# Optimization experiments

Measured on AMD Instinct MI355X. Metric: run time of the kernel, lower is better.

The kernel has to match this reference:

```python
import jax, jax.numpy as jnp
import numpy as np

E = 8          # num_experts
D = 512        # embed_dim
FF = 4         # ff_mult
H = D * FF     # hidden
B, N = 4, 2048
TOP_K = 2


def setup_inputs() -> dict:
    key = jax.random.key(0)
    ks = jax.random.split(key, 6)
    tokens = jax.random.normal(ks[0], (B, N, D), dtype=jnp.float32)
    # token-choice top-k routing: logits -> top-2 experts per token
    logits = jax.random.normal(ks[1], (B, N, E), dtype=jnp.float32)
    topv, topi = jax.lax.top_k(logits, TOP_K)            # (B,N,K)
    disp = jnp.zeros((B, N, E), jnp.float32)
    disp = jnp.take_along_axis(disp, topi, axis=-1)  # placeholder shape trick avoided below
    disp = jnp.zeros((B, N, E), jnp.float32).at[
        jnp.arange(B)[:, None, None], jnp.arange(N)[None, :, None], topi
    ].set(1.0)                                            # (B,N,E) 0/1 dispatch mask
    w = jax.nn.softmax(topv, axis=-1)                     # combine weights over selected
    comb = jnp.zeros((B, N, E), jnp.float32).at[
        jnp.arange(B)[:, None, None], jnp.arange(N)[None, :, None], topi
    ].set(w)
    # expert params (xavier-ish scale); out_proj gain 0.02 as in module init
    Wg = jax.random.normal(ks[2], (E, D, H), dtype=jnp.float32) * (2.0 / (D + H)) ** 0.5
    Wv = jax.random.normal(ks[3], (E, D, H), dtype=jnp.float32) * (2.0 / (D + H)) ** 0.5
    Wo = jax.random.normal(ks[4], (E, H, D), dtype=jnp.float32) * 0.02 * (2.0 / (D + H)) ** 0.5
    scales = jnp.full((E,), 1.0 / E, dtype=jnp.float32)   # output_scale per expert
    return {"tokens": tokens, "dispatch_weights": disp, "combine_weights": comb,
            "Wg": Wg, "Wv": Wv, "Wo": Wo, "scales": scales}


def reference(tokens, dispatch_weights, combine_weights, Wg, Wv, Wo, scales):
    """ExpertPool.forward: per-expert SwiGLU FFN, combined by routing weights.

    Dense-masked formulation (same math as gather->FFN->weighted scatter-add:
    expert outputs only contribute where dispatch>0).
    """
    b, n, d = tokens.shape
    x = tokens.reshape(b * n, d)                          # (M, D)
    gate = jax.nn.gelu(jnp.einsum('md,edh->emh', x, Wg), approximate=False)
    value = jnp.einsum('md,edh->emh', x, Wv)
    out_e = jnp.einsum('emh,ehd->emd', gate * value, Wo) * scales[:, None, None]
    mask = dispatch_weights.reshape(b * n, -1) > 0        # (M, E)
    w = jnp.where(mask, combine_weights.reshape(b * n, -1), 0.0)
    out = jnp.einsum('emd,me->md', out_e, w)              # weighted combine
    return out.reshape(b, n, d)
```

## Files before the change

### kernel.cpp

```cpp
#include <hip/hip_runtime.h>
#include <hip/hip_bf16.h>


#define NEXP 8
#define DIM 512
#define HID 2048
#define MTOK 8192
#define PMAX (2*MTOK)
#define TM 128
#define MT 144

typedef __bf16 bf16;
typedef __bf16 bf16x8 __attribute__((ext_vector_type(8)));
typedef float  f32x4  __attribute__((ext_vector_type(4)));

#define WAITVM(N) asm volatile("s_waitcnt vmcnt(" #N ")" ::: "memory")
#define SCHED0    __builtin_amdgcn_sched_barrier(0)
#define BAR       __builtin_amdgcn_s_barrier

__device__ __forceinline__ void gload16(const bf16* g, bf16* l) {
  __builtin_amdgcn_global_load_lds(
      (const __attribute__((address_space(1))) void*)g,
      (__attribute__((address_space(3))) void*)l, 16, 0, 0);
}

__device__ __forceinline__ float gelu_f(float x){
  float s = x * 0.70710678118654752f;
  float a = fabsf(s);
  float t = 1.0f / fmaf(0.3275911f, a, 1.0f);
  float p = t*(0.254829592f + t*(-0.284496736f + t*(1.421413741f +
            t*(-1.453152027f + t*1.061405429f))));
  float er = 1.0f - p*__expf(-s*s);
  er = copysignf(er, s);
  return 0.5f*x*(1.0f + er);
}

__device__ __forceinline__ bool tile_map(const int* __restrict__ cnt, int T,
                                         int& row0, int& nrows) {
  int sb = 0, stt = 0; bool ok = false;
#pragma unroll
  for (int q=0; q<NEXP; q++){
    int c = cnt[q];
    int nt = (c + TM-1)/TM;
    if (!ok && T >= stt && T < stt+nt){
      int k = T - stt;
      row0 = sb + k*TM;
      int nr = c - k*TM; if (nr > TM) nr = TM;
      nrows = nr; ok = true;
    }
    stt += nt; sb += c;
  }
  return ok;
}

__global__ __launch_bounds__(256) void k_prep(
    const float* __restrict__ Wg, const float* __restrict__ Wv,
    const float* __restrict__ Wo,
    bf16* __restrict__ WgT, bf16* __restrict__ WvT, bf16* __restrict__ WoT,
    const float* __restrict__ disp, int* __restrict__ cnt) {
  __shared__ __align__(16) bf16 t[64][72];
  __shared__ int lc[NEXP];
  const int b = blockIdx.x, tid = threadIdx.x;

  if (b < 6144) {
    const float* pin; bf16* pout; int R, C, c0, r0;
    if (b < 4096) {
      int u = b;
      int bx = u&31, by = (u>>5)&7, z = u>>8;
      int e = z & (NEXP-1);
      pin  = ((z < NEXP) ? Wg : Wv) + (size_t)e*DIM*HID;
      pout = ((z < NEXP) ? WgT : WvT) + (size_t)e*DIM*HID;
      R = DIM; C = HID; c0 = bx*64; r0 = by*64;
    } else {
      int u = b - 4096;
      int bx = u&7, by = (u>>3)&31, z = u>>8;
      pin  = Wo  + (size_t)z*HID*DIM;
      pout = WoT + (size_t)z*HID*DIM;
      R = HID; C = DIM; c0 = bx*64; r0 = by*64;
    }
    {
      const int rr = tid>>4, cc4 = (tid&15)*4;
#pragma unroll
      for (int i=0;i<4;i++){
        int r = i*16 + rr;
        float4 v = *(const float4*)&pin[(size_t)(r0+r)*C + c0 + cc4];
        t[cc4+0][r]=(bf16)v.x; t[cc4+1][r]=(bf16)v.y;
        t[cc4+2][r]=(bf16)v.z; t[cc4+3][r]=(bf16)v.w;
      }
    }
    __syncthreads();
    {
      const int rr8 = tid>>3, cc8 = (tid&7)*8;
#pragma unroll
      for (int i=0;i<2;i++){
        int c = i*32 + rr8;
        *(uint4*)&pout[(size_t)(c0+c)*R + r0 + cc8] = *(const uint4*)&t[c][cc8];
      }
    }
    return;
  }
  {
    if (tid < NEXP) lc[tid] = 0;
    __syncthreads();
    int m = (b - 6144)*256 + tid;
    float4 d0 = *(const float4*)&disp[(size_t)m*NEXP];
    float4 d1 = *(const float4*)&disp[(size_t)m*NEXP+4];
    if (d0.x>0.f) atomicAdd(&lc[0],1);
    if (d0.y>0.f) atomicAdd(&lc[1],1);
    if (d0.z>0.f) atomicAdd(&lc[2],1);
    if (d0.w>0.f) atomicAdd(&lc[3],1);
    if (d1.x>0.f) atomicAdd(&lc[4],1);
    if (d1.y>0.f) atomicAdd(&lc[5],1);
    if (d1.z>0.f) atomicAdd(&lc[6],1);
    if (d1.w>0.f) atomicAdd(&lc[7],1);
    __syncthreads();
    if (tid < NEXP) atomicAdd(&cnt[tid], lc[tid]);
  }
}

__global__ __launch_bounds__(256) void k_fill(const float* __restrict__ disp,
    const float* __restrict__ comb, const float* __restrict__ scales,
    const float* __restrict__ tokens, const int* __restrict__ cnt,
    int* __restrict__ fillc, float* __restrict__ sw, int* __restrict__ sslot,
    bf16* __restrict__ Xg) {
  __shared__ int sl[64];
  const int tid = threadIdx.x;
  if (tid < 32){
    int m = blockIdx.x*32 + tid;
    int base[NEXP]; int b = 0;
#pragma unroll
    for (int e=0;e<NEXP;e++){ base[e] = b; b += cnt[e]; }
    int jj = 0;
#pragma unroll
    for (int e=0;e<NEXP;e++){
      float dv = disp[(size_t)m*NEXP + e];
      if (dv > 0.f) {
        int s = atomicAdd(&fillc[e], 1);
        int g = base[e] + s;
        sw[g] = comb[(size_t)m*NEXP + e] * scales[e];
        if (jj < 2){ sslot[m*2 + jj] = g; sl[tid*2 + jj] = g; }
        jj++;
      }
    }
  }
  __syncthreads();
  for (int t=0; t<32; t++){
    int m = blockIdx.x*32 + t;
    float2 v = *(const float2*)&tokens[(size_t)m*DIM + tid*2];
    bf16 o[2]; o[0]=(bf16)v.x; o[1]=(bf16)v.y;
    unsigned u = *(unsigned*)o;
    int g0 = sl[t*2], g1 = sl[t*2+1];
    *(unsigned*)&Xg[(size_t)g0*DIM + tid*2] = u;
    *(unsigned*)&Xg[(size_t)g1*DIM + tid*2] = u;
  }
}

__global__ __launch_bounds__(256) void k_gemm1(const bf16* __restrict__ Xg,
    const bf16* __restrict__ WgT, const bf16* __restrict__ WvT,
    const int* __restrict__ cnt, bf16* __restrict__ H1) {
  int row0, nrows;
  if (!tile_map(cnt, blockIdx.y, row0, nrows)) return;
  const int n0 = blockIdx.x*64;
  __shared__ __align__(16) bf16 Al[2*128*32];
  __shared__ __align__(16) bf16 Bgl[2*64*32];
  __shared__ __align__(16) bf16 Bvl[2*64*32];
  const int tid = threadIdx.x, lane = tid&63;
  const int wr = (tid>>7)&1, wc = (tid>>6)&1;
  int eb = 0, e = 0;
#pragma unroll
  for (int q=0;q<NEXP;q++){ if (row0 >= eb) e = q; eb += cnt[q]; }
  {
    int b2 = 0;
#pragma unroll
    for (int q=0;q<NEXP;q++){ if (row0 >= b2 && row0 < b2+cnt[q]) e = q; b2 += cnt[q]; }
  }
  const bf16* __restrict__ wg = WgT + (size_t)e*HID*DIM;
  const bf16* __restrict__ wv = WvT + (size_t)e*HID*DIM;

  const bf16* asrc[2];
#pragma unroll
  for (int i=0;i<2;i++){
    int c = i*256 + tid;
    int r = c>>2, qs = (c&3) ^ ((r>>1)&3);
    int gr = (r < nrows) ? (row0 + r) : row0;
    asrc[i] = Xg + (size_t)gr*DIM + qs*8;
  }
  const bf16 *bsg, *bsv;
  {
    int r = tid>>2, qs = (tid&3) ^ ((r>>1)&3);
    size_t o = (size_t)(n0 + r)*DIM + qs*8;
    bsg = wg + o; bsv = wv + o;
  }
  const int wbase = (tid&192)*8;

  auto stage = [&](int bi, int kt){
    const int k0 = kt*32;
    gload16(asrc[0]+k0, Al + bi*4096 + wbase);
    gload16(asrc[1]+k0, Al + bi*4096 + 2048 + wbase);
    gload16(bsg+k0, Bgl + bi*2048 + wbase);
    gload16(bsv+k0, Bvl + bi*2048 + wbase);
  };

  f32x4 accg[4][2] = {}, accv[4][2] = {};
  const int r15 = lane&15;
  const int koff = ((lane>>4) ^ ((r15>>1)&3))*8;
  stage(0, 0);
  for (int kt=0; kt<DIM/32; ++kt){
    const int bi = kt&1;
    if (kt+1 < DIM/32){ stage(bi^1, kt+1); WAITVM(4); }
    else WAITVM(0);
    BAR(); SCHED0;
    bf16x8 a[4], bg[2], bv[2];
#pragma unroll
    for (int ni=0; ni<2; ni++){
      bg[ni] = *(const bf16x8*)&Bgl[bi*2048 + (wc*32 + ni*16 + r15)*32 + koff];
      bv[ni] = *(const bf16x8*)&Bvl[bi*2048 + (wc*32 + ni*16 + r15)*32 + koff];
    }
#pragma unroll
    for (int mi=0; mi<4; mi++)
      a[mi] = *(const bf16x8*)&Al[bi*4096 + (wr*64 + mi*16 + r15)*32 + koff];
#pragma unroll
    for (int mi=0; mi<4; mi++)
#pragma unroll
      for (int ni=0; ni<2; ni++){
        accg[mi][ni] = __builtin_amdgcn_mfma_f32_16x16x32_bf16(a[mi], bg[ni], accg[mi][ni], 0,0,0);
        accv[mi][ni] = __builtin_amdgcn_mfma_f32_16x16x32_bf16(a[mi], bv[ni], accv[mi][ni], 0,0,0);
      }
    BAR(); SCHED0;
  }
  const int cb = n0 + wc*32 + r15;
  const int rb = wr*64 + (lane>>4)*4;
#pragma unroll
  for (int mi=0; mi<4; mi++)
#pragma unroll
    for (int j=0; j<4; j++){
      int r = rb + mi*16 + j;
      if (r < nrows){
#pragma unroll
        for (int ni=0; ni<2; ni++){
          float g = accg[mi][ni][j], v = accv[mi][ni][j];
          H1[(size_t)(row0+r)*HID + cb + ni*16] = (bf16)(gelu_f(g)*v);
        }
      }
    }
}

__global__ __launch_bounds__(256) void k_gemm2(const bf16* __restrict__ H1,
    const bf16* __restrict__ WoT, const int* __restrict__ cnt,
    const float* __restrict__ sw, bf16* __restrict__ gout) {
  const int L = blockIdx.x;
  const int T = (L&7)*18 + (L>>5);
  const int n0 = ((L>>3)&3)*128;
  int row0, nrows;
  if (!tile_map(cnt, T, row0, nrows)) return;
  __shared__ __align__(16) bf16 Al[2*128*32];
  __shared__ __align__(16) bf16 Bl[2*128*32];
  const int tid = threadIdx.x, lane = tid&63;
  const int wr = (tid>>7)&1, wc = (tid>>6)&1;
  int e = 0;
  {
    int b2 = 0;
#pragma unroll
    for (int q=0;q<NEXP;q++){ if (row0 >= b2 && row0 < b2+cnt[q]) e = q; b2 += cnt[q]; }
  }
  const bf16* __restrict__ wo = WoT + (size_t)e*DIM*HID;

  const bf16 *asrc[2], *bsrc[2];
#pragma unroll
  for (int i=0;i<2;i++){
    int c = i*256 + tid;
    int r = c>>2, qs = (c&3) ^ ((r>>1)&3);
    int ar = (r < nrows) ? (row0 + r) : row0;
    asrc[i] = H1 + (size_t)ar*HID + qs*8;
    bsrc[i] = wo + (size_t)(n0 + r)*HID + qs*8;
  }
  const int wbase = (tid&192)*8;

  auto stage = [&](int bi, int kt){
    const int k0 = kt*32;
#pragma unroll
    for (int i=0;i<2;i++){
      gload16(asrc[i]+k0, Al + bi*4096 + i*2048 + wbase);
      gload16(bsrc[i]+k0, Bl + bi*4096 + i*2048 + wbase);
    }
  };

  f32x4 acc[4][4] = {};
  const int r15 = lane&15;
  const int koff = ((lane>>4) ^ ((r15>>1)&3))*8;
  stage(0, 0);
  for (int kt=0; kt<HID/32; ++kt){
    const int bi = kt&1;
    if (kt+1 < HID/32){ stage(bi^1, kt+1); WAITVM(4); }
    else WAITVM(0);
    BAR(); SCHED0;
    bf16x8 a[4], b[4];
#pragma unroll
    for (int ni=0; ni<4; ni++)
      b[ni] = *(const bf16x8*)&Bl[bi*4096 + (wc*64 + ni*16 + r15)*32 + koff];
#pragma unroll
    for (int mi=0; mi<4; mi++)
      a[mi] = *(const bf16x8*)&Al[bi*4096 + (wr*64 + mi*16 + r15)*32 + koff];
#pragma unroll
    for (int mi=0; mi<4; mi++)
#pragma unroll
      for (int ni=0; ni<4; ni++)
        acc[mi][ni] = __builtin_amdgcn_mfma_f32_16x16x32_bf16(a[mi], b[ni], acc[mi][ni], 0,0,0);
    BAR(); SCHED0;
  }
  const int cb = n0 + wc*64 + r15;
  const int rb = wr*64 + (lane>>4)*4;
#pragma unroll
  for (int mi=0; mi<4; mi++)
#pragma unroll
    for (int j=0; j<4; j++){
      int r = rb + mi*16 + j;
      if (r < nrows){
        int slot = row0 + r;
        float wgt = sw[slot];
        bf16* op = gout + (size_t)slot*DIM + cb;
#pragma unroll
        for (int ni=0; ni<4; ni++)
          op[ni*16] = (bf16)(acc[mi][ni][j] * wgt);
      }
    }
}

__global__ __launch_bounds__(256) void k_comb(const bf16* __restrict__ gout,
    const int* __restrict__ sslot, float* __restrict__ out) {
  int idx = blockIdx.x*256 + threadIdx.x;
  int m = idx >> 7, c4 = (idx & 127)*4;
  int s0 = sslot[m*2], s1 = sslot[m*2+1];
  const bf16* p0 = gout + (size_t)s0*DIM + c4;
  const bf16* p1 = gout + (size_t)s1*DIM + c4;
  bf16 a0[4], a1[4];
  *(uint2*)a0 = *(const uint2*)p0;
  *(uint2*)a1 = *(const uint2*)p1;
  float4 x;
  x.x = (float)a0[0] + (float)a1[0];
  x.y = (float)a0[1] + (float)a1[1];
  x.z = (float)a0[2] + (float)a1[2];
  x.w = (float)a0[3] + (float)a1[3];
  *(float4*)&out[(size_t)m*DIM + c4] = x;
}

extern "C" void kernel_launch(void* const* d_in, const int* in_sizes, int n_in,
                              void* d_out, int out_size, void* d_ws, size_t ws_size,
                              hipStream_t stream) {
  const float* tokens = (const float*)d_in[0];
  const float* disp   = (const float*)d_in[1];
  const float* comb   = (const float*)d_in[2];
  const float* Wg     = (const float*)d_in[3];
  const float* Wv     = (const float*)d_in[4];
  const float* Wo     = (const float*)d_in[5];
  const float* scales = (const float*)d_in[6];
  float* out = (float*)d_out;

  size_t off = 0;
  char* wsb = (char*)d_ws;
  auto take = [&](size_t bytes)->char* {
    char* q = wsb + off; off += (bytes + 255) & ~(size_t)255; return q;
  };
  int*   cnt   = (int*)  take(NEXP*4);
  int*   fillc = (int*)  take(NEXP*4);
  float* sw    = (float*)take((size_t)PMAX*4);
  int*   sslot = (int*)  take((size_t)MTOK*2*4);
  bf16*  Xg    = (bf16*) take((size_t)PMAX*DIM*2);
  bf16*  WgT   = (bf16*) take((size_t)NEXP*DIM*HID*2);
  bf16*  WvT   = (bf16*) take((size_t)NEXP*DIM*HID*2);
  bf16*  WoT   = (bf16*) take((size_t)NEXP*DIM*HID*2);
  bf16*  H1    = (bf16*) take((size_t)PMAX*HID*2);
  bf16*  gout  = WgT;
  (void)ws_size; (void)in_sizes; (void)n_in; (void)out_size;

  hipMemsetAsync(d_ws, 0, 512, stream);

  k_prep <<<dim3(6176), 256, 0, stream>>>(Wg, Wv, Wo, WgT, WvT, WoT, disp, cnt);
  k_fill <<<dim3(MTOK/32), 256, 0, stream>>>(disp, comb, scales, tokens, cnt,
                                             fillc, sw, sslot, Xg);
  k_gemm1<<<dim3(HID/64, MT), 256, 0, stream>>>(Xg, WgT, WvT, cnt, H1);
  k_gemm2<<<dim3(8*18*4), 256, 0, stream>>>(H1, WoT, cnt, sw, gout);
  k_comb <<<dim3(MTOK*DIM/4/256), 256, 0, stream>>>(gout, sslot, out);
}
```

Before: 219.1 us.

## Gather tokens by index in GEMM1 instead of materializing a permuted copy

Token conversion to bf16 moves into the prep kernel as a dense, coalesced pass. The fill kernel now records only a slot-to-token index. GEMM1 then reads A rows indirectly through that index rather than from a pre-scattered, duplicated Xg buffer. This drops the scatter write of 16K rows and shrinks k_fill to a tiny routing pass, at the cost of one extra index load per A row in GEMM1.

```diff
diff --git a/kernel.cpp b/kernel.cpp
--- a/kernel.cpp
+++ b/kernel.cpp
@@ -53,7 +53,15 @@
   return ok;
 }
 
-__global__ __launch_bounds__(256) void k_prep(
+__device__ __forceinline__ int expert_of(const int* __restrict__ cnt, int row0){
+  int e = 0, b2 = 0;
+#pragma unroll
+  for (int q=0;q<NEXP;q++){ if (row0 >= b2 && row0 < b2+cnt[q]) e = q; b2 += cnt[q]; }
+  return e;
+}
+
+__global__ __launch_bounds__(256) void k_prep(const float* __restrict__ tokens,
+    bf16* __restrict__ Xb,
     const float* __restrict__ Wg, const float* __restrict__ Wv,
     const float* __restrict__ Wo,
     bf16* __restrict__ WgT, bf16* __restrict__ WvT, bf16* __restrict__ WoT,
@@ -62,17 +70,25 @@
   __shared__ int lc[NEXP];
   const int b = blockIdx.x, tid = threadIdx.x;
 
-  if (b < 6144) {
+  if (b < 4096) {
+    int i = b*256 + tid;
+    float4 v = ((const float4* __restrict__)tokens)[i];
+    bf16 o[4];
+    o[0]=(bf16)v.x; o[1]=(bf16)v.y; o[2]=(bf16)v.z; o[3]=(bf16)v.w;
+    *(uint2*)&Xb[(size_t)i*4] = *(uint2*)o;
+    return;
+  }
+  if (b < 10240) {
     const float* pin; bf16* pout; int R, C, c0, r0;
-    if (b < 4096) {
-      int u = b;
+    if (b < 8192) {
+      int u = b - 4096;
       int bx = u&31, by = (u>>5)&7, z = u>>8;
       int e = z & (NEXP-1);
       pin  = ((z < NEXP) ? Wg : Wv) + (size_t)e*DIM*HID;
       pout = ((z < NEXP) ? WgT : WvT) + (size_t)e*DIM*HID;
       R = DIM; C = HID; c0 = bx*64; r0 = by*64;
     } else {
-      int u = b - 4096;
+      int u = b - 8192;
       int bx = u&7, by = (u>>3)&31, z = u>>8;
       pin  = Wo  + (size_t)z*HID*DIM;
       pout = WoT + (size_t)z*HID*DIM;
@@ -102,7 +118,7 @@
   {
     if (tid < NEXP) lc[tid] = 0;
     __syncthreads();
-    int m = (b - 6144)*256 + tid;
+    int m = (b - 10240)*256 + tid;
     float4 d0 = *(const float4*)&disp[(size_t)m*NEXP];
     float4 d1 = *(const float4*)&disp[(size_t)m*NEXP+4];
     if (d0.x>0.f) atomicAdd(&lc[0],1);
@@ -120,60 +136,40 @@
 
 __global__ __launch_bounds__(256) void k_fill(const float* __restrict__ disp,
     const float* __restrict__ comb, const float* __restrict__ scales,
-    const float* __restrict__ tokens, const int* __restrict__ cnt,
-    int* __restrict__ fillc, float* __restrict__ sw, int* __restrict__ sslot,
-    bf16* __restrict__ Xg) {
-  __shared__ int sl[64];
-  const int tid = threadIdx.x;
-  if (tid < 32){
-    int m = blockIdx.x*32 + tid;
-    int base[NEXP]; int b = 0;
-#pragma unroll
-    for (int e=0;e<NEXP;e++){ base[e] = b; b += cnt[e]; }
-    int jj = 0;
-#pragma unroll
-    for (int e=0;e<NEXP;e++){
-      float dv = disp[(size_t)m*NEXP + e];
-      if (dv > 0.f) {
-        int s = atomicAdd(&fillc[e], 1);
-        int g = base[e] + s;
-        sw[g] = comb[(size_t)m*NEXP + e] * scales[e];
-        if (jj < 2){ sslot[m*2 + jj] = g; sl[tid*2 + jj] = g; }
-        jj++;
-      }
-    }
-  }
-  __syncthreads();
-  for (int t=0; t<32; t++){
-    int m = blockIdx.x*32 + t;
-    float2 v = *(const float2*)&tokens[(size_t)m*DIM + tid*2];
-    bf16 o[2]; o[0]=(bf16)v.x; o[1]=(bf16)v.y;
-    unsigned u = *(unsigned*)o;
-    int g0 = sl[t*2], g1 = sl[t*2+1];
-    *(unsigned*)&Xg[(size_t)g0*DIM + tid*2] = u;
-    *(unsigned*)&Xg[(size_t)g1*DIM + tid*2] = u;
-  }
-}
-
-__global__ __launch_bounds__(256) void k_gemm1(const bf16* __restrict__ Xg,
+    const int* __restrict__ cnt, int* __restrict__ fillc,
+    int* __restrict__ stok, float* __restrict__ sw, int* __restrict__ sslot) {
+  int m = blockIdx.x*256 + threadIdx.x;
+  int base[NEXP]; int b = 0;
+#pragma unroll
+  for (int e=0;e<NEXP;e++){ base[e] = b; b += cnt[e]; }
+  int jj = 0;
+#pragma unroll
+  for (int e=0;e<NEXP;e++){
+    float dv = disp[(size_t)m*NEXP + e];
+    if (dv > 0.f) {
+      int s = atomicAdd(&fillc[e], 1);
+      int g = base[e] + s;
+      stok[g] = m;
+      sw[g] = comb[(size_t)m*NEXP + e] * scales[e];
+      if (jj < 2) sslot[m*2 + jj] = g;
+      jj++;
+    }
+  }
+}
+
+__global__ __launch_bounds__(256) void k_gemm1(const bf16* __restrict__ Xb,
     const bf16* __restrict__ WgT, const bf16* __restrict__ WvT,
-    const int* __restrict__ cnt, bf16* __restrict__ H1) {
+    const int* __restrict__ cnt, const int* __restrict__ stok,
+    bf16* __restrict__ H1) {
   int row0, nrows;
   if (!tile_map(cnt, blockIdx.y, row0, nrows)) return;
+  const int e = expert_of(cnt, row0);
   const int n0 = blockIdx.x*64;
   __shared__ __align__(16) bf16 Al[2*128*32];
   __shared__ __align__(16) bf16 Bgl[2*64*32];
   __shared__ __align__(16) bf16 Bvl[2*64*32];
   const int tid = threadIdx.x, lane = tid&63;
   const int wr = (tid>>7)&1, wc = (tid>>6)&1;
-  int eb = 0, e = 0;
-#pragma unroll
-  for (int q=0;q<NEXP;q++){ if (row0 >= eb) e = q; eb += cnt[q]; }
-  {
-    int b2 = 0;
-#pragma unroll
-    for (int q=0;q<NEXP;q++){ if (row0 >= b2 && row0 < b2+cnt[q]) e = q; b2 += cnt[q]; }
-  }
   const bf16* __restrict__ wg = WgT + (size_t)e*HID*DIM;
   const bf16* __restrict__ wv = WvT + (size_t)e*HID*DIM;
 
@@ -183,7 +179,7 @@
     int c = i*256 + tid;
     int r = c>>2, qs = (c&3) ^ ((r>>1)&3);
     int gr = (r < nrows) ? (row0 + r) : row0;
-    asrc[i] = Xg + (size_t)gr*DIM + qs*8;
+    asrc[i] = Xb + (size_t)stok[gr]*DIM + qs*8;
   }
   const bf16 *bsg, *bsv;
   {
@@ -253,16 +249,11 @@
   const int n0 = ((L>>3)&3)*128;
   int row0, nrows;
   if (!tile_map(cnt, T, row0, nrows)) return;
+  const int e = expert_of(cnt, row0);
   __shared__ __align__(16) bf16 Al[2*128*32];
   __shared__ __align__(16) bf16 Bl[2*128*32];
   const int tid = threadIdx.x, lane = tid&63;
   const int wr = (tid>>7)&1, wc = (tid>>6)&1;
-  int e = 0;
-  {
-    int b2 = 0;
-#pragma unroll
-    for (int q=0;q<NEXP;q++){ if (row0 >= b2 && row0 < b2+cnt[q]) e = q; b2 += cnt[q]; }
-  }
   const bf16* __restrict__ wo = WoT + (size_t)e*DIM*HID;
 
   const bf16 *asrc[2], *bsrc[2];
@@ -363,9 +354,10 @@
   };
   int*   cnt   = (int*)  take(NEXP*4);
   int*   fillc = (int*)  take(NEXP*4);
+  int*   stok  = (int*)  take((size_t)PMAX*4);
   float* sw    = (float*)take((size_t)PMAX*4);
   int*   sslot = (int*)  take((size_t)MTOK*2*4);
-  bf16*  Xg    = (bf16*) take((size_t)PMAX*DIM*2);
+  bf16*  Xb    = (bf16*) take((size_t)MTOK*DIM*2);
   bf16*  WgT   = (bf16*) take((size_t)NEXP*DIM*HID*2);
   bf16*  WvT   = (bf16*) take((size_t)NEXP*DIM*HID*2);
   bf16*  WoT   = (bf16*) take((size_t)NEXP*DIM*HID*2);
@@ -375,10 +367,11 @@
 
   hipMemsetAsync(d_ws, 0, 512, stream);
 
-  k_prep <<<dim3(6176), 256, 0, stream>>>(Wg, Wv, Wo, WgT, WvT, WoT, disp, cnt);
-  k_fill <<<dim3(MTOK/32), 256, 0, stream>>>(disp, comb, scales, tokens, cnt,
-                                             fillc, sw, sslot, Xg);
-  k_gemm1<<<dim3(HID/64, MT), 256, 0, stream>>>(Xg, WgT, WvT, cnt, H1);
+  k_prep <<<dim3(10272), 256, 0, stream>>>(tokens, Xb, Wg, Wv, Wo,
+                                           WgT, WvT, WoT, disp, cnt);
+  k_fill <<<dim3(MTOK/256), 256, 0, stream>>>(disp, comb, scales, cnt,
+                                              fillc, stok, sw, sslot);
+  k_gemm1<<<dim3(HID/64, MT), 256, 0, stream>>>(Xb, WgT, WvT, cnt, stok, H1);
   k_gemm2<<<dim3(8*18*4), 256, 0, stream>>>(H1, WoT, cnt, sw, gout);
   k_comb <<<dim3(MTOK*DIM/4/256), 256, 0, stream>>>(gout, sslot, out);
 }
```

New measurement: 203.8 us, median of 2. 7.0% less time.
